# Kernel tuning notes

Hardware: AMD Instinct MI355X
Metric: run time of the kernel (lower is better)

The kernel has to match this reference:

```python
import jax, jax.numpy as jnp
import numpy as np

N = 10000   # nodes per graph copy
E = 50000   # directed edges before to_undirected
B = 4       # batch size (graph is repeated B times)
K = 16      # num_neg + 1
D = 64      # in_dim == out_dim
R = 200     # num_relation (embedding table has 2R rows)
L = 3       # num_layer
NODE_RATIO = 0.1
DEGREE_RATIO = 1.0


def setup_inputs() -> dict:
    key = jax.random.key(0)
    ks = jax.random.split(key, 16)
    s = 0.05
    edge_index = jax.random.randint(ks[0], (2, E), 0, N, dtype=jnp.int32)
    edge_attr = jax.random.randint(ks[1], (E,), 0, R, dtype=jnp.int32)
    # asserts in source require h and r constant along the negative axis
    h_index = jnp.tile(jax.random.randint(ks[2], (B, 1), 0, N, dtype=jnp.int32), (1, K))
    r_index = jnp.tile(jax.random.randint(ks[3], (B, 1), 0, R, dtype=jnp.int32), (1, K))
    t_index = jax.random.randint(ks[4], (B, K), 0, N, dtype=jnp.int32)
    return {
        'h_index': h_index, 'r_index': r_index, 't_index': t_index,
        'hidden_states': jax.random.normal(ks[5], (B, D), jnp.float32),
        'rel_hidden_states': jax.random.normal(ks[6], (2 * R, D), jnp.float32),
        'edge_index': edge_index, 'edge_attr': edge_attr,
        'score_text_embs': jax.random.normal(ks[7], (N, D), jnp.float32) * 0.1,
        'all_index': jnp.arange(N, dtype=jnp.int32),
        'rel_emb_table': jax.random.normal(ks[8], (2 * R, D), jnp.float32) * s,
        'W_lin': jax.random.normal(ks[9], (2 * D, D), jnp.float32) * s,
        'b_lin': jnp.zeros((D,), jnp.float32),
        'W_mlp1': jax.random.normal(ks[10], (D, 2 * D), jnp.float32) * s,
        'b_mlp1': jnp.zeros((2 * D,), jnp.float32),
        'W_mlp2': jax.random.normal(ks[11], (2 * D, 1), jnp.float32) * s,
        'b_mlp2': jnp.zeros((1,), jnp.float32),
        'rel_w': 1.0 + jax.random.normal(ks[12], (L, 2 * R, D), jnp.float32) * s,
        'conv_W': jax.random.normal(ks[13], (L, 12 * D, D), jnp.float32) * s,
        'conv_b': jnp.zeros((L, D), jnp.float32),
    }


def _score(hidden, rel, W_lin, b_lin, W1, b1, W2, b2):
    # linear(cat[hidden, rel]) -> heuristic; mlp(hidden * heuristic) -> scalar
    heur = jnp.concatenate([hidden, rel], axis=-1) @ W_lin + b_lin
    x = hidden * heur
    h = jax.nn.relu(x @ W1 + b1)
    return (h @ W2 + b2)[..., 0]


def _forward(h_index, r_index, t_index, hidden_states, rel_hidden_states,
             edge_index, edge_attr, score_text_embs, all_index, rel_emb_table,
             W_lin, b_lin, W_mlp1, b_mlp1, W_mlp2, b_mlp2, rel_w, conv_W, conv_b):
    f32 = hidden_states.dtype
    # --- to_undirected: add reversed edges (edge_attr copied, as in PyG) ---
    ei = jnp.concatenate([edge_index, edge_index[::-1]], axis=1)      # [2, 2E]
    ea = jnp.concatenate([edge_attr, edge_attr])                       # [2E]
    E2 = 2 * E
    # --- _repeat_graph: B copies with node-index offsets ---
    offsets = jnp.arange(B, dtype=jnp.int32) * N
    ei_b = jnp.transpose(ei[None] + offsets[:, None, None], (1, 0, 2)).reshape(2, B * E2)
    ea_b = jnp.tile(ea, B)
    Nt, Et = B * N, B * E2
    src, dst = ei_b[0], ei_b[1]
    h0 = h_index[:, 0] + offsets                                       # [B]
    t_full = t_index + offsets[:, None]                                # [B, K]
    rel_embeds = rel_emb_table[r_index[:, 0]].astype(f32)              # [B, D]
    # --- init_input_embeds: tail text embeds then head embeds; score at heads ---
    input_embeds = jnp.zeros((Nt, D), f32).at[all_index].set(score_text_embs)
    input_embeds = input_embeds.at[h0].set(hidden_states)
    score = jnp.zeros((Nt,), f32).at[h0].set(
        _score(hidden_states, rel_embeds, W_lin, b_lin, W_mlp1, b_mlp1, W_mlp2, b_mlp2))
    query0 = rel_embeds[0]   # index_batch is all-zeros in source -> query[0] everywhere
    # --- pna degree mean over the full batched graph ---
    deg_in_full = jax.ops.segment_sum(jnp.ones((Et,), f32), dst, num_segments=Nt)
    pna_mean = jnp.mean(jnp.log(deg_in_full + 1.0))
    ks_n = max(1, int(NODE_RATIO * Nt))
    es = max(1, int(DEGREE_RATIO * ks_n * Et / Nt))
    hidden = input_embeds
    for l in range(L):
        # select_edges: top-ks nodes by score, then top-es outgoing edges
        thr = jax.lax.top_k(score, ks_n)[0][-1]
        s_src = score[src]
        edge_score = jnp.where(s_src >= thr, s_src, -jnp.inf)
        thr_e = jax.lax.top_k(edge_score, es)[0][-1]
        emask = (edge_score >= thr_e) & jnp.isfinite(edge_score)       # [Et]
        em = emask.astype(f32)
        # relation-conditioned messages gated by sigmoid(score of source)
        m = jax.nn.sigmoid(s_src)[:, None] * hidden[src] * rel_w[l][ea_b]
        mf = m * em[:, None]
        deg = jax.ops.segment_sum(em, dst, num_segments=Nt)            # [Nt]
        denom = jnp.maximum(deg, 1.0)[:, None]
        mean_a = jax.ops.segment_sum(mf, dst, num_segments=Nt) / denom
        sq = jax.ops.segment_sum(mf * mf, dst, num_segments=Nt) / denom
        std = jnp.sqrt(jnp.maximum(sq - mean_a * mean_a, 0.0) + 1e-6)
        mmax = jax.ops.segment_max(jnp.where(emask[:, None], m, -jnp.inf), dst, num_segments=Nt)
        mmin = jax.ops.segment_min(jnp.where(emask[:, None], m, jnp.inf), dst, num_segments=Nt)
        has = (deg > 0)[:, None]
        mmax = jnp.where(has, mmax, 0.0)
        mmin = jnp.where(has, mmin, 0.0)
        feat = jnp.concatenate([mean_a, mmax, mmin, std], axis=-1)     # [Nt, 4D]
        sc_log = jnp.log(deg + 1.0)
        amp = (sc_log / pna_mean)[:, None]
        att = (pna_mean / (sc_log + 1e-6))[:, None]
        feat_all = jnp.concatenate([feat, feat * amp, feat * att], -1)  # [Nt, 12D]
        upd = jax.nn.relu(feat_all @ conv_W[l] + conv_b[l])            # [Nt, D]
        out_deg = jax.ops.segment_sum(em, src, num_segments=Nt)
        omask = out_deg > 0
        hidden = jnp.where(omask[:, None], hidden + upd, hidden)
        new_score = _score(hidden, jnp.broadcast_to(query0, hidden.shape),
                           W_lin, b_lin, W_mlp1, b_mlp1, W_mlp2, b_mlp2)
        score = jnp.where(omask, new_score, score)
    return score[t_full]                                               # [B, K]


def reference(h_index, r_index, t_index, hidden_states, rel_hidden_states,
              edge_index, edge_attr, score_text_embs, all_index, rel_emb_table,
              W_lin, b_lin, W_mlp1, b_mlp1, W_mlp2, b_mlp2, rel_w, conv_W, conv_b):
    return _forward(h_index, r_index, t_index, hidden_states, rel_hidden_states,
                    edge_index, edge_attr, score_text_embs, all_index, rel_emb_table,
                    W_lin, b_lin, W_mlp1, b_mlp1, W_mlp2, b_mlp2, rel_w, conv_W, conv_b)
```

## Files before the change

### kernel.cpp

```cpp
#include <hip/hip_runtime.h>
#include <math.h>

#define N_NODES 10000
#define E_EDGES 50000
#define NT      40000
#define KS_N    4000
#define ES_E    40000
#define WTOT    400000u
#define CHUNK   16384
#define SEL_BLOCKS 40

__device__ __forceinline__ unsigned f2u(float f) {
    unsigned b = __float_as_uint(f);
    return (b & 0x80000000u) ? ~b : (b | 0x80000000u);
}
__device__ __forceinline__ float u2f(unsigned u) {
    unsigned b = (u & 0x80000000u) ? (u & 0x7fffffffu) : ~u;
    return __uint_as_float(b);
}
__device__ __forceinline__ float wave_sum64(float x) {
    for (int off = 32; off > 0; off >>= 1) x += __shfl_down(x, off, 64);
    return x;
}

__global__ void count_deg(const int* __restrict__ ei, unsigned* __restrict__ deg) {
    int j = blockIdx.x * 256 + threadIdx.x;
    if (j < E_EDGES) {
        atomicAdd(&deg[ei[j]], 1u);
        atomicAdd(&deg[ei[E_EDGES + j]], 1u);
    }
}

__global__ __launch_bounds__(1024) void scan_degrees(const unsigned* __restrict__ deg,
                                                     unsigned* __restrict__ rowptr,
                                                     unsigned* __restrict__ cursor) {
    __shared__ unsigned wsum[16];
    __shared__ unsigned carry;
    int tid = threadIdx.x, lane = tid & 63, w = tid >> 6;
    if (tid == 0) carry = 0;
    __syncthreads();
    for (int base = 0; base < N_NODES; base += 1024) {
        int i = base + tid;
        unsigned v = (i < N_NODES) ? deg[i] : 0u;
        unsigned x = v;
        for (int off = 1; off < 64; off <<= 1) {
            unsigned y = __shfl_up(x, off, 64);
            if (lane >= off) x += y;
        }
        if (lane == 63) wsum[w] = x;
        __syncthreads();
        if (tid < 16) {
            unsigned s = wsum[tid];
            for (int off = 1; off < 16; off <<= 1) {
                unsigned y = __shfl_up(s, off, 64);
                if (tid >= off) s += y;
            }
            wsum[tid] = s;
        }
        __syncthreads();
        unsigned woff = (w > 0) ? wsum[w - 1] : 0u;
        unsigned excl = carry + woff + x - v;
        if (i < N_NODES) { rowptr[i] = excl; cursor[i] = excl; }
        __syncthreads();
        if (tid == 0) carry += wsum[15];
        __syncthreads();
    }
    if (tid == 0) rowptr[N_NODES] = carry;
}

__global__ void scatter_edges(const int* __restrict__ ei, const int* __restrict__ ea,
                              unsigned* __restrict__ cursor, unsigned* __restrict__ inedge) {
    int j = blockIdx.x * 256 + threadIdx.x;
    if (j < E_EDGES) {
        unsigned s = (unsigned)ei[j];
        unsigned d = (unsigned)ei[E_EDGES + j];
        unsigned a = (unsigned)ea[j];
        unsigned p1 = atomicAdd(&cursor[d], 1u);
        inedge[p1] = s | (a << 16);
        unsigned p2 = atomicAdd(&cursor[s], 1u);
        inedge[p2] = d | (a << 16);
    }
}

__global__ __launch_bounds__(1024) void pna_kernel(const unsigned* __restrict__ degb,
                                                   float* __restrict__ scalars) {
    __shared__ float ws[16];
    int tid = threadIdx.x;
    float s = 0.0f;
    for (int i = tid; i < N_NODES; i += 1024) s += logf((float)degb[i] + 1.0f);
    for (int off = 32; off > 0; off >>= 1) s += __shfl_down(s, off, 64);
    if ((tid & 63) == 0) ws[tid >> 6] = s;
    __syncthreads();
    if (tid == 0) {
        float t = 0.0f;
        for (int i = 0; i < 16; ++i) t += ws[i];
        scalars[3] = t / (float)N_NODES;
    }
}

__global__ void init_hidden(const float* __restrict__ text, float* __restrict__ hidden) {
    int i = blockIdx.x * 256 + threadIdx.x;
    if (i < NT * 64) {
        int v = i >> 6;
        hidden[i] = (v < N_NODES) ? text[i] : 0.0f;
    }
}

__device__ float wave_score_g(float hid, float rel, const float* Wlin, const float* blin,
                              const float* W1, const float* b1, const float* W2, float b2v,
                              int lane) {
    float heur = blin[lane];
    for (int i = 0; i < 64; ++i) heur += __shfl(hid, i, 64) * Wlin[i * 64 + lane];
    for (int i = 0; i < 64; ++i) heur += __shfl(rel, i, 64) * Wlin[(64 + i) * 64 + lane];
    float x = hid * heur;
    float a0 = b1[lane], a1 = b1[64 + lane];
    for (int i = 0; i < 64; ++i) {
        float xv = __shfl(x, i, 64);
        a0 += xv * W1[i * 128 + lane];
        a1 += xv * W1[i * 128 + 64 + lane];
    }
    a0 = fmaxf(a0, 0.0f); a1 = fmaxf(a1, 0.0f);
    float part = a0 * W2[lane] + a1 * W2[64 + lane];
    part = wave_sum64(part);
    part = __shfl(part, 0, 64);
    return part + b2v;
}

__global__ void init_heads(const int* __restrict__ h_index, const int* __restrict__ r_index,
                           const float* __restrict__ hidden_states,
                           const float* __restrict__ rel_table,
                           const float* __restrict__ W_lin, const float* __restrict__ b_lin,
                           const float* __restrict__ W1, const float* __restrict__ b1,
                           const float* __restrict__ W2, const float* __restrict__ b2,
                           float* __restrict__ hidden, float* __restrict__ score,
                           float* __restrict__ qh) {
    __shared__ float q0[64];
    int tid = threadIdx.x, w = tid >> 6, lane = tid & 63;
    int b = w;
    int h0 = h_index[b * 16] + b * N_NODES;
    float hs  = hidden_states[b * 64 + lane];
    float rel = rel_table[r_index[b * 16] * 64 + lane];
    hidden[h0 * 64 + lane] = hs;
    if (b == 0) q0[lane] = rel;
    float s = wave_score_g(hs, rel, W_lin, b_lin, W1, b1, W2, b2[0], lane);
    if (lane == 0) score[h0] = s;
    __syncthreads();
    if (w == 0) {
        float acc = b_lin[lane];
        for (int i = 0; i < 64; ++i) acc += q0[i] * W_lin[(64 + i) * 64 + lane];
        qh[lane] = acc;
    }
}

__device__ void block_pick(unsigned h, unsigned r, unsigned* outd, unsigned* outr,
                           unsigned* scr) {
    int tid = threadIdx.x, lane = tid & 63, w = tid >> 6;
    __syncthreads();
    unsigned x = h;
    for (int off = 1; off < 64; off <<= 1) {
        unsigned y = __shfl_up(x, off, 64);
        if (lane >= off) x += y;
    }
    if (lane == 63) scr[w] = x;
    __syncthreads();
    unsigned woff = 0;
    for (int i = 0; i < 4; ++i) if (i < w) woff += scr[i];
    unsigned excl = woff + x - h;
    if (r >= excl && r < excl + h) { scr[4] = (unsigned)tid; scr[5] = r - excl; }
    __syncthreads();
    *outd = scr[4]; *outr = scr[5];
}

__global__ __launch_bounds__(256) void select_compact(
    const float* __restrict__ score, const unsigned* __restrict__ degb,
    unsigned* __restrict__ ghn, unsigned* __restrict__ ghw,
    unsigned* __restrict__ state, float* __restrict__ scalars,
    unsigned* __restrict__ countp, int* __restrict__ list,
    float* __restrict__ sigp, int rbase) {
    __shared__ unsigned lh[512];
    __shared__ unsigned scr[8];
    __shared__ unsigned sh_flag;
    __shared__ unsigned sh_state[4];
    int tid = threadIdx.x;
    unsigned pn = 0, pw = 0;
    unsigned rn = NT - KS_N, rw_ = WTOT - ES_E;
    for (int pass = 0; pass < 4; ++pass) {
        lh[tid] = 0; lh[256 + tid] = 0;
        __syncthreads();
        int shift = 24 - pass * 8;
        for (int v = blockIdx.x * 256 + tid; v < NT; v += SEL_BLOCKS * 256) {
            unsigned key = f2u(score[v]);
            unsigned wg = degb[v % N_NODES];
            unsigned dig = (key >> shift) & 255u;
            if (pass == 0) {
                atomicAdd(&lh[dig], 1u);
                if (wg) atomicAdd(&lh[256 + dig], wg);
            } else {
                unsigned hi = key >> (shift + 8);
                if (hi == pn) atomicAdd(&lh[dig], 1u);
                if (wg && hi == pw) atomicAdd(&lh[256 + dig], wg);
            }
        }
        __syncthreads();
        if (lh[tid]) atomicAdd(&ghn[tid], lh[tid]);
        if (lh[256 + tid]) atomicAdd(&ghw[tid], lh[256 + tid]);
        __threadfence();
        __syncthreads();
        if (tid == 0)
            sh_flag = (atomicAdd(&state[8], 1u) == SEL_BLOCKS - 1) ? 1u : 0u;
        __syncthreads();
        unsigned tgt = (unsigned)(rbase + pass + 1);
        if (sh_flag) {
            unsigned hn = atomicAdd(&ghn[tid], 0u);
            unsigned hw = atomicAdd(&ghw[tid], 0u);
            ghn[tid] = 0; ghw[tid] = 0;
            unsigned dn, rn2, dw, rw2;
            block_pick(hn, rn, &dn, &rn2, scr);
            block_pick(hw, rw_, &dw, &rw2, scr);
            if (tid == 0) {
                pn = (pn << 8) | dn;
                pw = (pw << 8) | dw;
                state[0] = pn; state[1] = rn2; state[2] = pw; state[3] = rw2;
                state[8] = 0;
                if (pass == 3) {
                    float thr = u2f(pn), thre = u2f(pw);
                    scalars[0] = thr;
                    scalars[1] = fmaxf(thr, thre);
                    *countp = 0;
                }
                __threadfence();
                atomicExch(&state[9], tgt);
            }
        }
        if (tid == 0) {
            while (atomicAdd(&state[9], 0u) < tgt) __builtin_amdgcn_s_sleep(8);
            sh_state[0] = atomicAdd(&state[0], 0u);
            sh_state[1] = atomicAdd(&state[1], 0u);
            sh_state[2] = atomicAdd(&state[2], 0u);
            sh_state[3] = atomicAdd(&state[3], 0u);
        }
        __syncthreads();
        pn = sh_state[0]; rn = sh_state[1]; pw = sh_state[2]; rw_ = sh_state[3];
    }
    float thr = u2f(pn);
    float THR = fmaxf(thr, u2f(pw));
    for (int v = blockIdx.x * 256 + tid; v < NT; v += SEL_BLOCKS * 256) {
        float sc = score[v];
        bool ok = sc >= THR;
        float sg = -1.0f;
        if (ok) sg = 1.0f / (1.0f + expf(-sc));
        sigp[v] = sg;
        if (ok && degb[v % N_NODES] > 0) {
            unsigned p = atomicAdd(countp, 1u);
            list[p] = v;
        }
    }
}

__global__ __launch_bounds__(256) void agg_feat(
    const float* __restrict__ sigp, const float* __restrict__ hidden,
    const unsigned* __restrict__ rowptr, const unsigned* __restrict__ inedge,
    const float* __restrict__ rel_w, const float* __restrict__ scalars,
    const unsigned* __restrict__ countp, const int* __restrict__ list,
    float* __restrict__ feat, float* __restrict__ ampatt, int layer,
    int mbase, int climit) {
    int count = (int)*countp;
    int cc = count - mbase; if (cc > climit) cc = climit;
    int tid = threadIdx.x, w = tid >> 6, lane = tid & 63;
    int li = blockIdx.x * 4 + w;
    if (li >= cc) return;
    int v = list[mbase + li];
    int b = v / N_NODES;
    int boff = b * N_NODES;
    int n = v - boff;
    const float* rw = rel_w + (size_t)layer * 400 * 64;
    unsigned r0 = rowptr[n], r1 = rowptr[n + 1];
    float sum = 0.f, sq = 0.f, mx = -INFINITY, mn = INFINITY;
    int cnt = 0;
    #pragma unroll 2
    for (unsigned e = r0; e < r1; ++e) {
        unsigned pk = inedge[e];
        int src = (int)(pk & 0xffffu) + boff;
        float sg = sigp[src];
        float h  = hidden[((size_t)src << 6) + lane];
        float rv = rw[((size_t)(pk >> 16) << 6) + lane];
        bool valid = sg >= 0.0f;
        float mval = sg * h * rv;
        if (valid) { sum += mval; sq += mval * mval; }
        mx = fmaxf(mx, valid ? mval : -INFINITY);
        mn = fminf(mn, valid ? mval : INFINITY);
        cnt += valid ? 1 : 0;
    }
    float denom = cnt > 0 ? (float)cnt : 1.0f;
    float mean = sum / denom;
    float sd = sqrtf(fmaxf(sq / denom - mean * mean, 0.0f) + 1e-6f);
    float* fr = feat + ((size_t)li << 8);
    fr[lane]        = mean;
    fr[64 + lane]   = cnt > 0 ? mx : 0.0f;
    fr[128 + lane]  = cnt > 0 ? mn : 0.0f;
    fr[192 + lane]  = sd;
    if (lane == 0) {
        float pna = scalars[3];
        float sl = logf((float)cnt + 1.0f);
        ampatt[li * 2]     = sl / pna;
        ampatt[li * 2 + 1] = pna / (sl + 1e-6f);
    }
}

#define FMA4(C, av, bv) { C[0] += av * bv.x; C[1] += av * bv.y; C[2] += av * bv.z; C[3] += av * bv.w; }

__global__ __launch_bounds__(256) void update_score(
    const float* __restrict__ conv_W, const float* __restrict__ conv_b,
    const unsigned* __restrict__ countp, const float* __restrict__ feat,
    const float* __restrict__ ampatt, float* __restrict__ hidden,
    float* __restrict__ score, const int* __restrict__ list,
    const float* __restrict__ W_lin, const float* __restrict__ qh,
    const float* __restrict__ W1, const float* __restrict__ b1,
    const float* __restrict__ W2, const float* __restrict__ b2,
    int layer, int mbase, int climit) {
    __shared__ float smem[32 * 34 + 32 * 196 + 64];
    float* sA   = smem;
    float* sB   = smem + 32 * 34;
    float* sAmp = smem + 32 * 34 + 32 * 196;
    float* sAtt = sAmp + 32;
    int count = (int)*countp;
    int cc = count - mbase; if (cc > climit) cc = climit;
    int m0 = blockIdx.x * 32;
    if (m0 >= cc) return;
    int tid = threadIdx.x;
    if (tid < 32) {
        int rl = m0 + tid;
        float a = 0.f, t = 0.f;
        if (rl < cc) { a = ampatt[rl * 2]; t = ampatt[rl * 2 + 1]; }
        sAmp[tid] = a; sAtt[tid] = t;
    }
    int mg = tid >> 4, ng = tid & 15, j0 = ng * 4;
    float c0[2][4] = {}, c1[2][4] = {}, c2[2][4] = {};
    const float* Wl = conv_W + (size_t)layer * 768 * 64;
    const float4* feat4 = (const float4*)feat;
    int arow = tid >> 3, akq = tid & 7;
    for (int k0 = 0; k0 < 256; k0 += 32) {
        __syncthreads();
        {
            float4 va = feat4[(((size_t)(m0 + arow)) << 6) + (k0 >> 2) + akq];
            sA[(akq * 4 + 0) * 34 + arow] = va.x;
            sA[(akq * 4 + 1) * 34 + arow] = va.y;
            sA[(akq * 4 + 2) * 34 + arow] = va.z;
            sA[(akq * 4 + 3) * 34 + arow] = va.w;
        }
        #pragma unroll
        for (int it = 0; it < 6; ++it) {
            int fi = it * 256 + tid;
            int rr = fi >> 4, q = fi & 15;
            int part = rr >> 5, kk = rr & 31;
            float4 vb = *(const float4*)(Wl + (((size_t)(part * 256 + k0 + kk)) << 6) + q * 4);
            float* d = &sB[kk * 196 + part * 64 + q * 4];
            d[0] = vb.x; d[1] = vb.y; d[2] = vb.z; d[3] = vb.w;
        }
        __syncthreads();
        #pragma unroll 4
        for (int kk = 0; kk < 32; ++kk) {
            float a0 = sA[kk * 34 + mg * 2];
            float a1 = sA[kk * 34 + mg * 2 + 1];
            float4 b0 = *(const float4*)&sB[kk * 196 + j0];
            float4 b1v = *(const float4*)&sB[kk * 196 + 64 + j0];
            float4 b2v = *(const float4*)&sB[kk * 196 + 128 + j0];
            FMA4(c0[0], a0, b0)  FMA4(c0[1], a1, b0)
            FMA4(c1[0], a0, b1v) FMA4(c1[1], a1, b1v)
            FMA4(c2[0], a0, b2v) FMA4(c2[1], a1, b2v)
        }
    }
    const float4 bias = *(const float4*)(conv_b + layer * 64 + j0);
    float4 o[2];
    #pragma unroll
    for (int mi = 0; mi < 2; ++mi) {
        int ml = mg * 2 + mi;
        float amp = sAmp[ml], att = sAtt[ml];
        o[mi].x = fmaxf(c0[mi][0] + amp * c1[mi][0] + att * c2[mi][0] + bias.x, 0.0f);
        o[mi].y = fmaxf(c0[mi][1] + amp * c1[mi][1] + att * c2[mi][1] + bias.y, 0.0f);
        o[mi].z = fmaxf(c0[mi][2] + amp * c1[mi][2] + att * c2[mi][2] + bias.z, 0.0f);
        o[mi].w = fmaxf(c0[mi][3] + amp * c1[mi][3] + att * c2[mi][3] + bias.w, 0.0f);
    }
    __syncthreads();
    float* sH = smem;
    float* sX = smem + 32 * 65;
    #pragma unroll
    for (int mi = 0; mi < 2; ++mi) {
        int ml = mg * 2 + mi;
        sH[ml * 65 + j0 + 0] = o[mi].x; sH[ml * 65 + j0 + 1] = o[mi].y;
        sH[ml * 65 + j0 + 2] = o[mi].z; sH[ml * 65 + j0 + 3] = o[mi].w;
    }
    __syncthreads();
    {
        int q = tid & 15, mB = tid >> 4;
        #pragma unroll
        for (int r = 0; r < 2; ++r) {
            int m = r * 16 + mB;
            int idx = m0 + m;
            if (idx < cc) {
                int v = list[mbase + idx];
                float4 hv = *(const float4*)&hidden[((size_t)v << 6) + q * 4];
                float h0 = hv.x + sH[m * 65 + q * 4 + 0];
                float h1 = hv.y + sH[m * 65 + q * 4 + 1];
                float h2 = hv.z + sH[m * 65 + q * 4 + 2];
                float h3 = hv.w + sH[m * 65 + q * 4 + 3];
                float4 hw = {h0, h1, h2, h3};
                *(float4*)&hidden[((size_t)v << 6) + q * 4] = hw;
                sH[m * 65 + q * 4 + 0] = h0; sH[m * 65 + q * 4 + 1] = h1;
                sH[m * 65 + q * 4 + 2] = h2; sH[m * 65 + q * 4 + 3] = h3;
            } else {
                sH[m * 65 + q * 4 + 0] = 0.f; sH[m * 65 + q * 4 + 1] = 0.f;
                sH[m * 65 + q * 4 + 2] = 0.f; sH[m * 65 + q * 4 + 3] = 0.f;
            }
        }
    }
    __syncthreads();
    const float4* Wl4 = (const float4*)W_lin;
    const float4* W14 = (const float4*)W1;
    {
        float4 qv = ((const float4*)qh)[ng];
        float acc[2][4];
        #pragma unroll
        for (int mi = 0; mi < 2; ++mi) {
            acc[mi][0] = qv.x; acc[mi][1] = qv.y; acc[mi][2] = qv.z; acc[mi][3] = qv.w;
        }
        for (int k = 0; k < 64; ++k) {
            float4 bv = Wl4[k * 16 + ng];
            #pragma unroll
            for (int mi = 0; mi < 2; ++mi) {
                float av = sH[(mg * 2 + mi) * 65 + k];
                acc[mi][0] += av * bv.x; acc[mi][1] += av * bv.y;
                acc[mi][2] += av * bv.z; acc[mi][3] += av * bv.w;
            }
        }
        #pragma unroll
        for (int mi = 0; mi < 2; ++mi) {
            int m = mg * 2 + mi;
            #pragma unroll
            for (int ni = 0; ni < 4; ++ni)
                sX[m * 65 + j0 + ni] = sH[m * 65 + j0 + ni] * acc[mi][ni];
        }
    }
    __syncthreads();
    {
        float4 bA = ((const float4*)b1)[ng], bB = ((const float4*)b1)[16 + ng];
        float accA[2][4], accB[2][4];
        #pragma unroll
        for (int mi = 0; mi < 2; ++mi) {
            accA[mi][0] = bA.x; accA[mi][1] = bA.y; accA[mi][2] = bA.z; accA[mi][3] = bA.w;
            accB[mi][0] = bB.x; accB[mi][1] = bB.y; accB[mi][2] = bB.z; accB[mi][3] = bB.w;
        }
        for (int k = 0; k < 64; ++k) {
            float4 bvA = W14[k * 32 + ng];
            float4 bvB = W14[k * 32 + 16 + ng];
            #pragma unroll
            for (int mi = 0; mi < 2; ++mi) {
                float av = sX[(mg * 2 + mi) * 65 + k];
                accA[mi][0] += av * bvA.x; accA[mi][1] += av * bvA.y;
                accA[mi][2] += av * bvA.z; accA[mi][3] += av * bvA.w;
                accB[mi][0] += av * bvB.x; accB[mi][1] += av * bvB.y;
                accB[mi][2] += av * bvB.z; accB[mi][3] += av * bvB.w;
            }
        }
        float4 w2A = ((const float4*)W2)[ng], w2B = ((const float4*)W2)[16 + ng];
        #pragma unroll
        for (int mi = 0; mi < 2; ++mi) {
            int m = mg * 2 + mi;
            float pA0 = fmaxf(accA[mi][0], 0.f), pB0 = fmaxf(accB[mi][0], 0.f);
            float pA1 = fmaxf(accA[mi][1], 0.f), pB1 = fmaxf(accB[mi][1], 0.f);
            float pA2 = fmaxf(accA[mi][2], 0.f), pB2 = fmaxf(accB[mi][2], 0.f);
            float pA3 = fmaxf(accA[mi][3], 0.f), pB3 = fmaxf(accB[mi][3], 0.f);
            sH[m * 65 + j0 + 0] = pA0 * w2A.x + pB0 * w2B.x;
            sH[m * 65 + j0 + 1] = pA1 * w2A.y + pB1 * w2B.y;
            sH[m * 65 + j0 + 2] = pA2 * w2A.z + pB2 * w2B.z;
            sH[m * 65 + j0 + 3] = pA3 * w2A.w + pB3 * w2B.w;
        }
    }
    __syncthreads();
    {
        float b2v = b2[0];
        int w = tid >> 6, lane = tid & 63;
        #pragma unroll 4
        for (int t = 0; t < 8; ++t) {
            int m = w * 8 + t;
            float p = sH[m * 65 + lane];
            float s = wave_sum64(p);
            if (lane == 0 && (m0 + m) < cc)
                score[list[mbase + m0 + m]] = s + b2v;
        }
    }
}

__global__ void gather_out(const float* __restrict__ score, const int* __restrict__ t_index,
                           float* __restrict__ out) {
    int i = threadIdx.x;
    int b = i >> 4;
    out[i] = score[t_index[i] + b * N_NODES];
}

extern "C" void kernel_launch(void* const* d_in, const int* in_sizes, int n_in,
                              void* d_out, int out_size, void* d_ws, size_t ws_size,
                              hipStream_t stream) {
    const int*   h_index       = (const int*)d_in[0];
    const int*   r_index       = (const int*)d_in[1];
    const int*   t_index       = (const int*)d_in[2];
    const float* hidden_states = (const float*)d_in[3];
    const int*   edge_index    = (const int*)d_in[5];
    const int*   edge_attr     = (const int*)d_in[6];
    const float* text          = (const float*)d_in[7];
    const float* rel_table     = (const float*)d_in[9];
    const float* W_lin         = (const float*)d_in[10];
    const float* b_lin         = (const float*)d_in[11];
    const float* W1            = (const float*)d_in[12];
    const float* b1            = (const float*)d_in[13];
    const float* W2            = (const float*)d_in[14];
    const float* b2            = (const float*)d_in[15];
    const float* rel_w         = (const float*)d_in[16];
    const float* conv_W        = (const float*)d_in[17];
    const float* conv_b        = (const float*)d_in[18];

    auto layout_bytes = [](size_t fch) -> size_t {
        auto al = [](size_t x) { return (x + 255) & ~(size_t)255; };
        size_t o = 0;
        o += al(256) * 3;
        o += al(1024) * 2;
        o += al((size_t)NT * 4);
        o += al((size_t)N_NODES * 4);
        o += al(256);
        o += al((size_t)NT * 4);
        o += al((size_t)NT * 64 * 4);
        o += al(fch * 256 * 4);
        o += al(fch * 2 * 4);
        o += al((size_t)NT * 4);
        o += al((size_t)(N_NODES + 1) * 4);
        o += al((size_t)N_NODES * 4);
        o += al((size_t)2 * E_EDGES * 4);
        return o;
    };
    const size_t FCH = (layout_bytes(NT) <= ws_size) ? (size_t)NT : (size_t)CHUNK;
    const int NCH = (FCH == (size_t)NT) ? 1 : 3;

    char* ws = (char*)d_ws;
    size_t off = 0;
    auto carve = [&](size_t bytes) -> char* {
        char* p = ws + off;
        off = (off + bytes + 255) & ~(size_t)255;
        return p;
    };
    float*    scalars = (float*)carve(256);
    unsigned* state   = (unsigned*)carve(256);
    unsigned* countp  = (unsigned*)carve(256);
    unsigned* ghn     = (unsigned*)carve(1024);
    unsigned* ghw     = (unsigned*)carve(1024);
    float*    score   = (float*)carve((size_t)NT * 4);
    unsigned* degb    = (unsigned*)carve((size_t)N_NODES * 4);
    size_t zero_end = off;
    float*    qh      = (float*)carve(256);
    float*    sigp    = (float*)carve((size_t)NT * 4);
    float*    hidden  = (float*)carve((size_t)NT * 64 * 4);
    float*    feat    = (float*)carve(FCH * 256 * 4);
    float*    ampatt  = (float*)carve(FCH * 2 * 4);
    int*      list    = (int*)carve((size_t)NT * 4);
    unsigned* rowptr  = (unsigned*)carve((size_t)(N_NODES + 1) * 4);
    unsigned* cursor  = (unsigned*)carve((size_t)N_NODES * 4);
    unsigned* inedge  = (unsigned*)carve((size_t)2 * E_EDGES * 4);
    if (off > ws_size) return;

    hipMemsetAsync(ws, 0, zero_end, stream);

    count_deg<<<(E_EDGES + 255) / 256, 256, 0, stream>>>(edge_index, degb);
    scan_degrees<<<1, 1024, 0, stream>>>(degb, rowptr, cursor);
    scatter_edges<<<(E_EDGES + 255) / 256, 256, 0, stream>>>(edge_index, edge_attr, cursor, inedge);
    pna_kernel<<<1, 1024, 0, stream>>>(degb, scalars);
    init_hidden<<<(NT * 64 + 255) / 256, 256, 0, stream>>>(text, hidden);
    init_heads<<<1, 256, 0, stream>>>(h_index, r_index, hidden_states, rel_table,
                                      W_lin, b_lin, W1, b1, W2, b2, hidden, score, qh);

    const int climit  = (int)FCH;
    const int aggGrid = climit / 4;
    const int updGrid = climit / 32;
    for (int l = 0; l < 3; ++l) {
        select_compact<<<SEL_BLOCKS, 256, 0, stream>>>(score, degb, ghn, ghw, state,
                                                       scalars, countp, list, sigp, l * 4);
        for (int c = 0; c < NCH; ++c) {
            int mbase = c * climit;
            agg_feat<<<aggGrid, 256, 0, stream>>>(sigp, hidden, rowptr, inedge, rel_w,
                                                  scalars, countp, list, feat, ampatt,
                                                  l, mbase, climit);
            update_score<<<updGrid, 256, 0, stream>>>(conv_W, conv_b, countp, feat, ampatt,
                                                      hidden, score, list, W_lin, qh,
                                                      W1, b1, W2, b2, l, mbase, climit);
        }
    }
    gather_out<<<1, 64, 0, stream>>>(score, t_index, (float*)d_out);
}
```

Before: 397.2 us.

## Fuse neighbor aggregation into update kernel with double-buffered hidden state

Merges the per-node aggregation kernel into the conv/score update kernel, so the aggregated 256-wide features stay in shared memory and are never written to or read back from global memory. To avoid read-after-write hazards between blocks, hidden state is double-buffered and a full device-to-device copy of the old hidden buffer is issued each layer. The block grows to 512 threads, and only half of them take part in the conv matmul. The extra 10 MB copy per layer and the lower matmul utilisation offset part of the traffic saved.

```diff
diff --git a/kernel.cpp b/kernel.cpp
--- a/kernel.cpp
+++ b/kernel.cpp
@@ -7,7 +7,6 @@
 #define KS_N    4000
 #define ES_E    40000
 #define WTOT    400000u
-#define CHUNK   16384
 #define SEL_BLOCKS 40
 
 __device__ __forceinline__ unsigned f2u(float f) {
@@ -257,100 +256,89 @@
     }
 }
 
-__global__ __launch_bounds__(256) void agg_feat(
-    const float* __restrict__ sigp, const float* __restrict__ hidden,
+#define FMA4(C, av, bv) { C[0] += av * bv.x; C[1] += av * bv.y; C[2] += av * bv.z; C[3] += av * bv.w; }
+
+__global__ __launch_bounds__(512) void update_fused(
+    const float* __restrict__ sigp, const float* __restrict__ hold,
+    float* __restrict__ hnew,
     const unsigned* __restrict__ rowptr, const unsigned* __restrict__ inedge,
     const float* __restrict__ rel_w, const float* __restrict__ scalars,
     const unsigned* __restrict__ countp, const int* __restrict__ list,
-    float* __restrict__ feat, float* __restrict__ ampatt, int layer,
-    int mbase, int climit) {
-    int count = (int)*countp;
-    int cc = count - mbase; if (cc > climit) cc = climit;
-    int tid = threadIdx.x, w = tid >> 6, lane = tid & 63;
-    int li = blockIdx.x * 4 + w;
-    if (li >= cc) return;
-    int v = list[mbase + li];
-    int b = v / N_NODES;
-    int boff = b * N_NODES;
-    int n = v - boff;
-    const float* rw = rel_w + (size_t)layer * 400 * 64;
-    unsigned r0 = rowptr[n], r1 = rowptr[n + 1];
-    float sum = 0.f, sq = 0.f, mx = -INFINITY, mn = INFINITY;
-    int cnt = 0;
-    #pragma unroll 2
-    for (unsigned e = r0; e < r1; ++e) {
-        unsigned pk = inedge[e];
-        int src = (int)(pk & 0xffffu) + boff;
-        float sg = sigp[src];
-        float h  = hidden[((size_t)src << 6) + lane];
-        float rv = rw[((size_t)(pk >> 16) << 6) + lane];
-        bool valid = sg >= 0.0f;
-        float mval = sg * h * rv;
-        if (valid) { sum += mval; sq += mval * mval; }
-        mx = fmaxf(mx, valid ? mval : -INFINITY);
-        mn = fminf(mn, valid ? mval : INFINITY);
-        cnt += valid ? 1 : 0;
-    }
-    float denom = cnt > 0 ? (float)cnt : 1.0f;
-    float mean = sum / denom;
-    float sd = sqrtf(fmaxf(sq / denom - mean * mean, 0.0f) + 1e-6f);
-    float* fr = feat + ((size_t)li << 8);
-    fr[lane]        = mean;
-    fr[64 + lane]   = cnt > 0 ? mx : 0.0f;
-    fr[128 + lane]  = cnt > 0 ? mn : 0.0f;
-    fr[192 + lane]  = sd;
-    if (lane == 0) {
-        float pna = scalars[3];
-        float sl = logf((float)cnt + 1.0f);
-        ampatt[li * 2]     = sl / pna;
-        ampatt[li * 2 + 1] = pna / (sl + 1e-6f);
-    }
-}
-
-#define FMA4(C, av, bv) { C[0] += av * bv.x; C[1] += av * bv.y; C[2] += av * bv.z; C[3] += av * bv.w; }
-
-__global__ __launch_bounds__(256) void update_score(
     const float* __restrict__ conv_W, const float* __restrict__ conv_b,
-    const unsigned* __restrict__ countp, const float* __restrict__ feat,
-    const float* __restrict__ ampatt, float* __restrict__ hidden,
-    float* __restrict__ score, const int* __restrict__ list,
+    float* __restrict__ score,
     const float* __restrict__ W_lin, const float* __restrict__ qh,
     const float* __restrict__ W1, const float* __restrict__ b1,
     const float* __restrict__ W2, const float* __restrict__ b2,
-    int layer, int mbase, int climit) {
-    __shared__ float smem[32 * 34 + 32 * 196 + 64];
-    float* sA   = smem;
-    float* sB   = smem + 32 * 34;
-    float* sAmp = smem + 32 * 34 + 32 * 196;
-    float* sAtt = sAmp + 32;
+    int layer) {
+    __shared__ float smem[14656];
+    float* sF   = smem;
+    float* sB   = smem + 8320;
+    float* sAmp = smem + 14592;
+    float* sAtt = smem + 14624;
     int count = (int)*countp;
-    int cc = count - mbase; if (cc > climit) cc = climit;
+    int cc = count;
     int m0 = blockIdx.x * 32;
     if (m0 >= cc) return;
     int tid = threadIdx.x;
-    if (tid < 32) {
-        int rl = m0 + tid;
-        float a = 0.f, t = 0.f;
-        if (rl < cc) { a = ampatt[rl * 2]; t = ampatt[rl * 2 + 1]; }
-        sAmp[tid] = a; sAtt[tid] = t;
-    }
+    int w = tid >> 6, lane = tid & 63;
+
+    {
+        const float* rw = rel_w + (size_t)layer * 400 * 64;
+        float pna = scalars[3];
+        for (int t = 0; t < 4; ++t) {
+            int li = w * 4 + t;
+            int gi = m0 + li;
+            float* fr = sF + li * 260;
+            if (gi < cc) {
+                int v = list[gi];
+                int b = v / N_NODES;
+                int boff = b * N_NODES;
+                int n = v - boff;
+                unsigned r0 = rowptr[n], r1 = rowptr[n + 1];
+                float sum = 0.f, sq = 0.f, mx = -INFINITY, mn = INFINITY;
+                int cnt = 0;
+                #pragma unroll 4
+                for (unsigned e = r0; e < r1; ++e) {
+                    unsigned pk = inedge[e];
+                    int src = (int)(pk & 0xffffu) + boff;
+                    float sg = sigp[src];
+                    float h  = hold[((size_t)src << 6) + lane];
+                    float rv = rw[((size_t)(pk >> 16) << 6) + lane];
+                    bool valid = sg >= 0.0f;
+                    float mval = sg * h * rv;
+                    if (valid) { sum += mval; sq += mval * mval; }
+                    mx = fmaxf(mx, valid ? mval : -INFINITY);
+                    mn = fminf(mn, valid ? mval : INFINITY);
+                    cnt += valid ? 1 : 0;
+                }
+                float denom = cnt > 0 ? (float)cnt : 1.0f;
+                float mean = sum / denom;
+                float sd = sqrtf(fmaxf(sq / denom - mean * mean, 0.0f) + 1e-6f);
+                fr[lane]        = mean;
+                fr[64 + lane]   = cnt > 0 ? mx : 0.0f;
+                fr[128 + lane]  = cnt > 0 ? mn : 0.0f;
+                fr[192 + lane]  = sd;
+                if (lane == 0) {
+                    float sl = logf((float)cnt + 1.0f);
+                    sAmp[li] = sl / pna;
+                    sAtt[li] = pna / (sl + 1e-6f);
+                }
+            } else {
+                fr[lane] = 0.f; fr[64 + lane] = 0.f;
+                fr[128 + lane] = 0.f; fr[192 + lane] = 0.f;
+                if (lane == 0) { sAmp[li] = 0.f; sAtt[li] = 0.f; }
+            }
+        }
+    }
+
     int mg = tid >> 4, ng = tid & 15, j0 = ng * 4;
     float c0[2][4] = {}, c1[2][4] = {}, c2[2][4] = {};
     const float* Wl = conv_W + (size_t)layer * 768 * 64;
-    const float4* feat4 = (const float4*)feat;
-    int arow = tid >> 3, akq = tid & 7;
     for (int k0 = 0; k0 < 256; k0 += 32) {
         __syncthreads();
-        {
-            float4 va = feat4[(((size_t)(m0 + arow)) << 6) + (k0 >> 2) + akq];
-            sA[(akq * 4 + 0) * 34 + arow] = va.x;
-            sA[(akq * 4 + 1) * 34 + arow] = va.y;
-            sA[(akq * 4 + 2) * 34 + arow] = va.z;
-            sA[(akq * 4 + 3) * 34 + arow] = va.w;
-        }
         #pragma unroll
-        for (int it = 0; it < 6; ++it) {
-            int fi = it * 256 + tid;
+        for (int it = 0; it < 3; ++it) {
+            int fi = it * 512 + tid;
             int rr = fi >> 4, q = fi & 15;
             int part = rr >> 5, kk = rr & 31;
             float4 vb = *(const float4*)(Wl + (((size_t)(part * 256 + k0 + kk)) << 6) + q * 4);
@@ -358,135 +346,110 @@
             d[0] = vb.x; d[1] = vb.y; d[2] = vb.z; d[3] = vb.w;
         }
         __syncthreads();
-        #pragma unroll 4
-        for (int kk = 0; kk < 32; ++kk) {
-            float a0 = sA[kk * 34 + mg * 2];
-            float a1 = sA[kk * 34 + mg * 2 + 1];
-            float4 b0 = *(const float4*)&sB[kk * 196 + j0];
-            float4 b1v = *(const float4*)&sB[kk * 196 + 64 + j0];
-            float4 b2v = *(const float4*)&sB[kk * 196 + 128 + j0];
-            FMA4(c0[0], a0, b0)  FMA4(c0[1], a1, b0)
-            FMA4(c1[0], a0, b1v) FMA4(c1[1], a1, b1v)
-            FMA4(c2[0], a0, b2v) FMA4(c2[1], a1, b2v)
-        }
-    }
-    const float4 bias = *(const float4*)(conv_b + layer * 64 + j0);
+        if (tid < 256) {
+            #pragma unroll 4
+            for (int kk = 0; kk < 32; ++kk) {
+                float a0 = sF[(mg * 2) * 260 + k0 + kk];
+                float a1 = sF[(mg * 2 + 1) * 260 + k0 + kk];
+                float4 b0 = *(const float4*)&sB[kk * 196 + j0];
+                float4 b1v = *(const float4*)&sB[kk * 196 + 64 + j0];
+                float4 b2v = *(const float4*)&sB[kk * 196 + 128 + j0];
+                FMA4(c0[0], a0, b0)  FMA4(c0[1], a1, b0)
+                FMA4(c1[0], a0, b1v) FMA4(c1[1], a1, b1v)
+                FMA4(c2[0], a0, b2v) FMA4(c2[1], a1, b2v)
+            }
+        }
+    }
     float4 o[2];
-    #pragma unroll
-    for (int mi = 0; mi < 2; ++mi) {
-        int ml = mg * 2 + mi;
-        float amp = sAmp[ml], att = sAtt[ml];
-        o[mi].x = fmaxf(c0[mi][0] + amp * c1[mi][0] + att * c2[mi][0] + bias.x, 0.0f);
-        o[mi].y = fmaxf(c0[mi][1] + amp * c1[mi][1] + att * c2[mi][1] + bias.y, 0.0f);
-        o[mi].z = fmaxf(c0[mi][2] + amp * c1[mi][2] + att * c2[mi][2] + bias.z, 0.0f);
-        o[mi].w = fmaxf(c0[mi][3] + amp * c1[mi][3] + att * c2[mi][3] + bias.w, 0.0f);
-    }
-    __syncthreads();
-    float* sH = smem;
-    float* sX = smem + 32 * 65;
-    #pragma unroll
-    for (int mi = 0; mi < 2; ++mi) {
-        int ml = mg * 2 + mi;
-        sH[ml * 65 + j0 + 0] = o[mi].x; sH[ml * 65 + j0 + 1] = o[mi].y;
-        sH[ml * 65 + j0 + 2] = o[mi].z; sH[ml * 65 + j0 + 3] = o[mi].w;
-    }
-    __syncthreads();
-    {
-        int q = tid & 15, mB = tid >> 4;
-        #pragma unroll
-        for (int r = 0; r < 2; ++r) {
-            int m = r * 16 + mB;
-            int idx = m0 + m;
-            if (idx < cc) {
-                int v = list[mbase + idx];
-                float4 hv = *(const float4*)&hidden[((size_t)v << 6) + q * 4];
-                float h0 = hv.x + sH[m * 65 + q * 4 + 0];
-                float h1 = hv.y + sH[m * 65 + q * 4 + 1];
-                float h2 = hv.z + sH[m * 65 + q * 4 + 2];
-                float h3 = hv.w + sH[m * 65 + q * 4 + 3];
-                float4 hw = {h0, h1, h2, h3};
-                *(float4*)&hidden[((size_t)v << 6) + q * 4] = hw;
-                sH[m * 65 + q * 4 + 0] = h0; sH[m * 65 + q * 4 + 1] = h1;
-                sH[m * 65 + q * 4 + 2] = h2; sH[m * 65 + q * 4 + 3] = h3;
-            } else {
-                sH[m * 65 + q * 4 + 0] = 0.f; sH[m * 65 + q * 4 + 1] = 0.f;
-                sH[m * 65 + q * 4 + 2] = 0.f; sH[m * 65 + q * 4 + 3] = 0.f;
-            }
-        }
-    }
-    __syncthreads();
-    const float4* Wl4 = (const float4*)W_lin;
-    const float4* W14 = (const float4*)W1;
-    {
-        float4 qv = ((const float4*)qh)[ng];
-        float acc[2][4];
+    if (tid < 256) {
+        const float4 bias = *(const float4*)(conv_b + layer * 64 + j0);
         #pragma unroll
         for (int mi = 0; mi < 2; ++mi) {
-            acc[mi][0] = qv.x; acc[mi][1] = qv.y; acc[mi][2] = qv.z; acc[mi][3] = qv.w;
-        }
-        for (int k = 0; k < 64; ++k) {
-            float4 bv = Wl4[k * 16 + ng];
-            #pragma unroll
-            for (int mi = 0; mi < 2; ++mi) {
-                float av = sH[(mg * 2 + mi) * 65 + k];
-                acc[mi][0] += av * bv.x; acc[mi][1] += av * bv.y;
-                acc[mi][2] += av * bv.z; acc[mi][3] += av * bv.w;
-            }
-        }
+            int ml = mg * 2 + mi;
+            float amp = sAmp[ml], att = sAtt[ml];
+            o[mi].x = fmaxf(c0[mi][0] + amp * c1[mi][0] + att * c2[mi][0] + bias.x, 0.0f);
+            o[mi].y = fmaxf(c0[mi][1] + amp * c1[mi][1] + att * c2[mi][1] + bias.y, 0.0f);
+            o[mi].z = fmaxf(c0[mi][2] + amp * c1[mi][2] + att * c2[mi][2] + bias.z, 0.0f);
+            o[mi].w = fmaxf(c0[mi][3] + amp * c1[mi][3] + att * c2[mi][3] + bias.w, 0.0f);
+        }
+    }
+    __syncthreads();
+    float* sH = smem;
+    float* sX = smem + 8320;
+    if (tid < 256) {
         #pragma unroll
         for (int mi = 0; mi < 2; ++mi) {
             int m = mg * 2 + mi;
-            #pragma unroll
-            for (int ni = 0; ni < 4; ++ni)
-                sX[m * 65 + j0 + ni] = sH[m * 65 + j0 + ni] * acc[mi][ni];
-        }
+            int idx = m0 + m;
+            if (idx < cc) {
+                int v = list[idx];
+                float4 hv = *(const float4*)&hold[((size_t)v << 6) + j0];
+                float h0 = hv.x + o[mi].x;
+                float h1 = hv.y + o[mi].y;
+                float h2 = hv.z + o[mi].z;
+                float h3 = hv.w + o[mi].w;
+                float4 hw = {h0, h1, h2, h3};
+                *(float4*)&hnew[((size_t)v << 6) + j0] = hw;
+                sH[m * 65 + j0 + 0] = h0; sH[m * 65 + j0 + 1] = h1;
+                sH[m * 65 + j0 + 2] = h2; sH[m * 65 + j0 + 3] = h3;
+            } else {
+                sH[m * 65 + j0 + 0] = 0.f; sH[m * 65 + j0 + 1] = 0.f;
+                sH[m * 65 + j0 + 2] = 0.f; sH[m * 65 + j0 + 3] = 0.f;
+            }
+        }
+    }
+    __syncthreads();
+    const float4* Wl4 = (const float4*)W_lin;
+    const float4* W14 = (const float4*)W1;
+    int row = tid >> 4;
+    {
+        float4 qv = ((const float4*)qh)[ng];
+        float acc[4] = {qv.x, qv.y, qv.z, qv.w};
+        for (int k = 0; k < 64; ++k) {
+            float4 bv = Wl4[k * 16 + ng];
+            float av = sH[row * 65 + k];
+            acc[0] += av * bv.x; acc[1] += av * bv.y;
+            acc[2] += av * bv.z; acc[3] += av * bv.w;
+        }
+        #pragma unroll
+        for (int ni = 0; ni < 4; ++ni)
+            sX[row * 65 + j0 + ni] = sH[row * 65 + j0 + ni] * acc[ni];
     }
     __syncthreads();
     {
         float4 bA = ((const float4*)b1)[ng], bB = ((const float4*)b1)[16 + ng];
-        float accA[2][4], accB[2][4];
-        #pragma unroll
-        for (int mi = 0; mi < 2; ++mi) {
-            accA[mi][0] = bA.x; accA[mi][1] = bA.y; accA[mi][2] = bA.z; accA[mi][3] = bA.w;
-            accB[mi][0] = bB.x; accB[mi][1] = bB.y; accB[mi][2] = bB.z; accB[mi][3] = bB.w;
-        }
+        float accA[4] = {bA.x, bA.y, bA.z, bA.w};
+        float accB[4] = {bB.x, bB.y, bB.z, bB.w};
         for (int k = 0; k < 64; ++k) {
             float4 bvA = W14[k * 32 + ng];
             float4 bvB = W14[k * 32 + 16 + ng];
-            #pragma unroll
-            for (int mi = 0; mi < 2; ++mi) {
-                float av = sX[(mg * 2 + mi) * 65 + k];
-                accA[mi][0] += av * bvA.x; accA[mi][1] += av * bvA.y;
-                accA[mi][2] += av * bvA.z; accA[mi][3] += av * bvA.w;
-                accB[mi][0] += av * bvB.x; accB[mi][1] += av * bvB.y;
-                accB[mi][2] += av * bvB.z; accB[mi][3] += av * bvB.w;
-            }
+            float av = sX[row * 65 + k];
+            accA[0] += av * bvA.x; accA[1] += av * bvA.y;
+            accA[2] += av * bvA.z; accA[3] += av * bvA.w;
+            accB[0] += av * bvB.x; accB[1] += av * bvB.y;
+            accB[2] += av * bvB.z; accB[3] += av * bvB.w;
         }
         float4 w2A = ((const float4*)W2)[ng], w2B = ((const float4*)W2)[16 + ng];
-        #pragma unroll
-        for (int mi = 0; mi < 2; ++mi) {
-            int m = mg * 2 + mi;
-            float pA0 = fmaxf(accA[mi][0], 0.f), pB0 = fmaxf(accB[mi][0], 0.f);
-            float pA1 = fmaxf(accA[mi][1], 0.f), pB1 = fmaxf(accB[mi][1], 0.f);
-            float pA2 = fmaxf(accA[mi][2], 0.f), pB2 = fmaxf(accB[mi][2], 0.f);
-            float pA3 = fmaxf(accA[mi][3], 0.f), pB3 = fmaxf(accB[mi][3], 0.f);
-            sH[m * 65 + j0 + 0] = pA0 * w2A.x + pB0 * w2B.x;
-            sH[m * 65 + j0 + 1] = pA1 * w2A.y + pB1 * w2B.y;
-            sH[m * 65 + j0 + 2] = pA2 * w2A.z + pB2 * w2B.z;
-            sH[m * 65 + j0 + 3] = pA3 * w2A.w + pB3 * w2B.w;
-        }
+        float pA0 = fmaxf(accA[0], 0.f), pB0 = fmaxf(accB[0], 0.f);
+        float pA1 = fmaxf(accA[1], 0.f), pB1 = fmaxf(accB[1], 0.f);
+        float pA2 = fmaxf(accA[2], 0.f), pB2 = fmaxf(accB[2], 0.f);
+        float pA3 = fmaxf(accA[3], 0.f), pB3 = fmaxf(accB[3], 0.f);
+        __syncthreads();
+        sH[row * 65 + j0 + 0] = pA0 * w2A.x + pB0 * w2B.x;
+        sH[row * 65 + j0 + 1] = pA1 * w2A.y + pB1 * w2B.y;
+        sH[row * 65 + j0 + 2] = pA2 * w2A.z + pB2 * w2B.z;
+        sH[row * 65 + j0 + 3] = pA3 * w2A.w + pB3 * w2B.w;
     }
     __syncthreads();
     {
         float b2v = b2[0];
-        int w = tid >> 6, lane = tid & 63;
         #pragma unroll 4
-        for (int t = 0; t < 8; ++t) {
-            int m = w * 8 + t;
+        for (int t = 0; t < 4; ++t) {
+            int m = w * 4 + t;
             float p = sH[m * 65 + lane];
             float s = wave_sum64(p);
             if (lane == 0 && (m0 + m) < cc)
-                score[list[mbase + m0 + m]] = s + b2v;
+                score[list[m0 + m]] = s + b2v;
         }
     }
 }
@@ -519,27 +482,6 @@
     const float* conv_W        = (const float*)d_in[17];
     const float* conv_b        = (const float*)d_in[18];
 
-    auto layout_bytes = [](size_t fch) -> size_t {
-        auto al = [](size_t x) { return (x + 255) & ~(size_t)255; };
-        size_t o = 0;
-        o += al(256) * 3;
-        o += al(1024) * 2;
-        o += al((size_t)NT * 4);
-        o += al((size_t)N_NODES * 4);
-        o += al(256);
-        o += al((size_t)NT * 4);
-        o += al((size_t)NT * 64 * 4);
-        o += al(fch * 256 * 4);
-        o += al(fch * 2 * 4);
-        o += al((size_t)NT * 4);
-        o += al((size_t)(N_NODES + 1) * 4);
-        o += al((size_t)N_NODES * 4);
-        o += al((size_t)2 * E_EDGES * 4);
-        return o;
-    };
-    const size_t FCH = (layout_bytes(NT) <= ws_size) ? (size_t)NT : (size_t)CHUNK;
-    const int NCH = (FCH == (size_t)NT) ? 1 : 3;
-
     char* ws = (char*)d_ws;
     size_t off = 0;
     auto carve = [&](size_t bytes) -> char* {
@@ -557,9 +499,8 @@
     size_t zero_end = off;
     float*    qh      = (float*)carve(256);
     float*    sigp    = (float*)carve((size_t)NT * 4);
-    float*    hidden  = (float*)carve((size_t)NT * 64 * 4);
-    float*    feat    = (float*)carve(FCH * 256 * 4);
-    float*    ampatt  = (float*)carve(FCH * 2 * 4);
+    float*    hidA    = (float*)carve((size_t)NT * 64 * 4);
+    float*    hidB    = (float*)carve((size_t)NT * 64 * 4);
     int*      list    = (int*)carve((size_t)NT * 4);
     unsigned* rowptr  = (unsigned*)carve((size_t)(N_NODES + 1) * 4);
     unsigned* cursor  = (unsigned*)carve((size_t)N_NODES * 4);
@@ -572,25 +513,22 @@
     scan_degrees<<<1, 1024, 0, stream>>>(degb, rowptr, cursor);
     scatter_edges<<<(E_EDGES + 255) / 256, 256, 0, stream>>>(edge_index, edge_attr, cursor, inedge);
     pna_kernel<<<1, 1024, 0, stream>>>(degb, scalars);
-    init_hidden<<<(NT * 64 + 255) / 256, 256, 0, stream>>>(text, hidden);
+    init_hidden<<<(NT * 64 + 255) / 256, 256, 0, stream>>>(text, hidA);
     init_heads<<<1, 256, 0, stream>>>(h_index, r_index, hidden_states, rel_table,
-                                      W_lin, b_lin, W1, b1, W2, b2, hidden, score, qh);
-
-    const int climit  = (int)FCH;
-    const int aggGrid = climit / 4;
-    const int updGrid = climit / 32;
+                                      W_lin, b_lin, W1, b1, W2, b2, hidA, score, qh);
+
+    const size_t hbytes = (size_t)NT * 64 * 4;
+    float* hold = hidA;
+    float* hnew = hidB;
     for (int l = 0; l < 3; ++l) {
         select_compact<<<SEL_BLOCKS, 256, 0, stream>>>(score, degb, ghn, ghw, state,
                                                        scalars, countp, list, sigp, l * 4);
-        for (int c = 0; c < NCH; ++c) {
-            int mbase = c * climit;
-            agg_feat<<<aggGrid, 256, 0, stream>>>(sigp, hidden, rowptr, inedge, rel_w,
-                                                  scalars, countp, list, feat, ampatt,
-                                                  l, mbase, climit);
-            update_score<<<updGrid, 256, 0, stream>>>(conv_W, conv_b, countp, feat, ampatt,
-                                                      hidden, score, list, W_lin, qh,
-                                                      W1, b1, W2, b2, l, mbase, climit);
-        }
+        hipMemcpyAsync(hnew, hold, hbytes, hipMemcpyDeviceToDevice, stream);
+        update_fused<<<(NT + 31) / 32, 512, 0, stream>>>(sigp, hold, hnew, rowptr, inedge,
+                                                         rel_w, scalars, countp, list,
+                                                         conv_W, conv_b, score,
+                                                         W_lin, qh, W1, b1, W2, b2, l);
+        float* tmp = hold; hold = hnew; hnew = tmp;
     }
     gather_out<<<1, 64, 0, stream>>>(score, t_index, (float*)d_out);
 }
```

Measured after the change: 541.7 us. 1.36x slower.
